# Optimization experiments

Measured on AMD Instinct MI355X. Metric: run time of the kernel, lower is better.

Reference implementation:

```python
import jax, jax.numpy as jnp
import numpy as np

EPS = 1e-5
N = 2097152


def _bn(x, gamma, beta):
    # training-mode BatchNorm1d: biased batch stats over the batch dim
    mean = jnp.mean(x, axis=0)
    var = jnp.var(x, axis=0)
    return (x - mean) * jax.lax.rsqrt(var + EPS) * gamma + beta


def _block(x, W1, g, b, W2, b2):
    # Linear(no bias) -> BN -> ReLU -> Linear(bias)
    h = jax.nn.relu(_bn(x @ W1, g, b))
    return h @ W2 + b2


def setup_inputs() -> dict:
    key = jax.random.key(0)
    ks = jax.random.split(key, 32)
    i = iter(range(32))
    rn = lambda shape, s=0.1: (jax.random.normal(ks[next(i)], shape, dtype=jnp.float32) * s)
    d = {
        "rotation": jax.random.normal(ks[next(i)], (N, 9), dtype=jnp.float32),
        "transition": jax.random.normal(ks[next(i)], (N, 3), dtype=jnp.float32),
        # key net: 3->32 (no bias), BN32, 32->64
        "kW1": rn((3, 32)), "kg": jnp.ones(32), "kb": jnp.zeros(32),
        "kW2": rn((32, 64)), "kb2": rn((64,)),
        # query net: 9->32 (no bias), BN32, 32->64
        "qW1": rn((9, 32)), "qg": jnp.ones(32), "qb": jnp.zeros(32),
        "qW2": rn((32, 64)), "qb2": rn((64,)),
        # value net: 3->32 (no bias), BN32, 32->64
        "vW1": rn((3, 32)), "vg": jnp.ones(32), "vb": jnp.zeros(32),
        "vW2": rn((32, 64)), "vb2": rn((64,)),
        # decoder: 64->32(nb), BN32, ReLU, 32->16(nb), BN16, ReLU, 16->1(b), sigmoid
        "dW1": rn((64, 32)), "dg1": jnp.ones(32), "db1": jnp.zeros(32),
        "dW2": rn((32, 16)), "dg2": jnp.ones(16), "db2": jnp.zeros(16),
        "dW3": rn((16, 1)), "db3": rn((1,)),
    }
    return d


def reference(rotation, transition,
              kW1, kg, kb, kW2, kb2,
              qW1, qg, qb, qW2, qb2,
              vW1, vg, vb, vW2, vb2,
              dW1, dg1, db1, dW2, dg2, db2, dW3, db3):
    k = _block(transition, kW1, kg, kb, kW2, kb2)   # [N, 64]
    q = _block(rotation, qW1, qg, qb, qW2, qb2)     # [N, 64]
    v = _block(transition, vW1, vg, vb, vW2, vb2)   # [N, 64]
    attn = jax.nn.softmax(k * q, axis=-1) * v        # [N, 64]
    h = jax.nn.relu(_bn(attn @ dW1, dg1, db1))       # [N, 32]
    h = jax.nn.relu(_bn(h @ dW2, dg2, db2))          # [N, 16]
    out = jax.nn.sigmoid(h @ dW3 + db3)              # [N, 1]
    return out
```

## Files before the change

kernel.cpp:

```cpp
#include <hip/hip_runtime.h>

#define EPS 1e-5f
#define L2E 1.442695041f

typedef __attribute__((ext_vector_type(8))) short short8;
typedef __attribute__((ext_vector_type(4))) float f32x4;
#define MFMA16(a,b,c) __builtin_amdgcn_mfma_f32_16x16x32_bf16(a,b,c,0,0,0)

typedef float __attribute__((may_alias)) fal;
typedef unsigned short __attribute__((may_alias)) sal;
typedef unsigned int __attribute__((may_alias)) u32al;
typedef uint4 __attribute__((may_alias)) u4al;
typedef f32x4 __attribute__((may_alias)) f4al;

union U8 { short8 s; uint4 u; };

__device__ __forceinline__ float wred(float v){
#pragma unroll
  for(int m=32;m>=1;m>>=1) v += __shfl_xor(v,m,64);
  return v;
}

__device__ __forceinline__ unsigned short f2bf(float f){
  union{unsigned int i; float x;}v; v.x=f;
  unsigned int u=v.i;
  unsigned int r=(u + 0x7fffu + ((u>>16)&1u))>>16;
  return (unsigned short)r;
}
__device__ __forceinline__ unsigned cvtpk(float lo, float hi){
  unsigned r; asm("v_cvt_pk_bf16_f32 %0, %1, %2" : "=v"(r) : "v"(lo), "v"(hi)); return r;
}
__device__ __forceinline__ float bflo(unsigned int u){
  union{unsigned int i; float x;}v; v.i=u<<16; return v.x;
}
__device__ __forceinline__ float bfhi(unsigned int u){
  union{unsigned int i; float x;}v; v.i=u&0xffff0000u; return v.x;
}

__device__ __host__ __forceinline__ int kperm(int k){
  int g=k>>3, e=k&7;
  return (e<4) ? 4*g+e : 16+4*g+(e-4);
}
__device__ __host__ __forceinline__ int kpermD(int kg){
  int kc=kg>>5, kk=kg&31, gm=kk>>3, e=kk&7;
  return 16*(2*kc+(e>>2)) + 4*gm + (e&3);
}

__global__ __launch_bounds__(256) void kT(const float* __restrict__ kW2, const float* __restrict__ qW2,
                                          const float* __restrict__ vW2, const float* __restrict__ dW1,
                                          const float* __restrict__ dW2,
                                          unsigned short* __restrict__ wbf){
  for(int idx=threadIdx.x; idx<2048; idx+=256){
    int k=idx&31, c=idx>>5;
    int f=kperm(k);
    wbf[c*32+k]       = f2bf(kW2[f*64+c]);
    wbf[2048+c*32+k]  = f2bf(qW2[f*64+c]);
    wbf[4096+c*32+k]  = f2bf(vW2[f*64+c]);
  }
  for(int idx=threadIdx.x; idx<2048; idx+=256){
    int f=idx&31, kg=idx>>5;
    wbf[6144 + f*64 + kg] = f2bf(dW1[kpermD(kg)*32 + f]);
  }
  for(int idx=threadIdx.x; idx<512; idx+=256){
    int k=idx>>4, f=idx&15;
    wbf[8192 + f*32 + k] = f2bf(dW2[idx]);
  }
}

__global__ __launch_bounds__(256) void kA(const float* __restrict__ rot, const float* __restrict__ tra,
                                          float* __restrict__ pA, int N){
  float a[63];
#pragma unroll
  for(int i=0;i<63;i++) a[i]=0.f;
  int stride = gridDim.x*blockDim.x;
  for(int row=blockIdx.x*blockDim.x+threadIdx.x; row<N; row+=stride){
    float t[3], r[9];
#pragma unroll
    for(int i=0;i<3;i++) t[i]=tra[row*3+i];
#pragma unroll
    for(int i=0;i<9;i++) r[i]=rot[row*9+i];
#pragma unroll
    for(int i=0;i<3;i++) a[i]+=t[i];
#pragma unroll
    for(int i=0;i<3;i++)
#pragma unroll
      for(int j=i;j<3;j++) a[3 + i*3 - (i*(i-1))/2 + (j-i)] += t[i]*t[j];
#pragma unroll
    for(int i=0;i<9;i++) a[9+i]+=r[i];
#pragma unroll
    for(int i=0;i<9;i++)
#pragma unroll
      for(int j=i;j<9;j++) a[18 + i*9 - (i*(i-1))/2 + (j-i)] += r[i]*r[j];
  }
#pragma unroll
  for(int i=0;i<63;i++) a[i]=wred(a[i]);
  __shared__ __align__(16) float lds[4][63];
  int wave=threadIdx.x>>6, lane=threadIdx.x&63;
  if(lane==0){
#pragma unroll
    for(int i=0;i<63;i++) lds[wave][i]=a[i];
  }
  __syncthreads();
  int t=threadIdx.x;
  if(t<63) pA[t*gridDim.x + blockIdx.x] = lds[0][t]+lds[1][t]+lds[2][t]+lds[3][t];
}

__global__ __launch_bounds__(256) void kA2(const float* __restrict__ pA, int nb,
    const float* __restrict__ kW1, const float* __restrict__ kg, const float* __restrict__ kb,
    const float* __restrict__ qW1, const float* __restrict__ qg, const float* __restrict__ qb,
    const float* __restrict__ vW1, const float* __restrict__ vg, const float* __restrict__ vb,
    float* __restrict__ cst, unsigned short* __restrict__ wA, float invN){
  __shared__ __align__(16) float tmp[63][4];
  __shared__ __align__(16) float mom[63];
  __shared__ __align__(16) float sSc[96];
  __shared__ __align__(16) float sBi[96];
  int t=threadIdx.x;
  if(t<252){
    int f=t>>2, q=t&3;
    int per=nb/4;
    float s=0.f;
    for(int i=0;i<per;i++) s+=pA[f*nb + q*per + i];
    tmp[f][q]=s;
  }
  __syncthreads();
  if(t<63) mom[t]=tmp[t][0]+tmp[t][1]+tmp[t][2]+tmp[t][3];
  __syncthreads();
  if(t<96){
    int net=t>>5, j=t&31;
    const float* W1; const float* g; const float* b; int din, sbase, mbase, obase;
    if(net==0){W1=kW1;g=kg;b=kb;din=3;sbase=0;mbase=3;obase=0;}
    else if(net==1){W1=qW1;g=qg;b=qb;din=9;sbase=9;mbase=18;obase=64;}
    else {W1=vW1;g=vg;b=vb;din=3;sbase=0;mbase=3;obase=128;}
    float mean=0.f, ex2=0.f;
    for(int i=0;i<din;i++){
      float wi=W1[i*32+j];
      mean += mom[sbase+i]*wi;
      int rowb = mbase + i*din - (i*(i-1))/2;
      for(int i2=i;i2<din;i2++){
        float w2=W1[i2*32+j];
        float m=mom[rowb + (i2-i)];
        ex2 += ((i2==i)?1.f:2.f)*wi*w2*m;
      }
    }
    mean*=invN; ex2*=invN;
    float var=ex2-mean*mean;
    float sc=g[j]*rsqrtf(var+EPS);
    float bi=b[j]-mean*sc;
    cst[obase+j]=sc; cst[obase+32+j]=bi;
    sSc[net*32+j]=sc; sBi[net*32+j]=bi;
  }
  __syncthreads();
  for(int i=threadIdx.x; i<3072; i+=256){
    int frag=i>>9, m=(i>>5)&15, k=i&31;
    int net=frag>>1, half=frag&1;
    int f = half*16+m;
    float v=0.f;
    if(net==0){
      if(k<3) v=kW1[k*32+f]*sSc[f];
      else if(k==3) v=sBi[f];
    } else if(net==1){
      if(k>=4 && k<13) v=qW1[(k-4)*32+f]*sSc[32+f];
      else if(k==3) v=sBi[32+f];
    } else {
      if(k<3) v=vW1[k*32+f]*sSc[64+f];
      else if(k==3) v=sBi[64+f];
    }
    wA[i]=f2bf(v);
  }
}

__global__ __launch_bounds__(256) void kRed(const float* __restrict__ part, int nf, int nb,
    const float* __restrict__ g, const float* __restrict__ b, float* __restrict__ cstOut, float invN){
  int f=blockIdx.x;
  float s1=0.f,s2=0.f;
  for(int i=threadIdx.x;i<nb;i+=256){ s1+=part[f*nb+i]; s2+=part[(nf+f)*nb+i]; }
  s1=wred(s1); s2=wred(s2);
  __shared__ __align__(16) float l1[4],l2[4];
  int wave=threadIdx.x>>6;
  if((threadIdx.x&63)==0){l1[wave]=s1;l2[wave]=s2;}
  __syncthreads();
  if(threadIdx.x==0){
    float a=l1[0]+l1[1]+l1[2]+l1[3];
    float c=l2[0]+l2[1]+l2[2]+l2[3];
    float mean=a*invN;
    float var=c*invN-mean*mean;
    float sc=g[f]*rsqrtf(var+EPS);
    float bi=b[f]-mean*sc;
    cstOut[f]=sc; cstOut[nf+f]=bi;
  }
}

__global__ __launch_bounds__(256) void kHeavyM(
    const float* __restrict__ rot, const float* __restrict__ tra,
    const unsigned short* __restrict__ wA, const unsigned short* __restrict__ wbf,
    const float* __restrict__ kb2, const float* __restrict__ qb2, const float* __restrict__ vb2,
    unsigned short* __restrict__ y1o, float* __restrict__ pB, int N, int nb4)
{
  __shared__ __align__(16) unsigned short sbK[2048];
  __shared__ __align__(16) unsigned short sbQ[2048];
  __shared__ __align__(16) unsigned short sbV[2048];
  __shared__ __align__(16) unsigned short sbD[2048];
  __shared__ __align__(16) unsigned short sA[3072];
  __shared__ __align__(16) sal ybuf[4][640];
  for(int i=threadIdx.x;i<2048;i+=256){
    int e=i&7;
    int rK=i>>5, clK=(i>>3)&3;
    int dK = rK*32 + ((clK^(rK&3))<<3) + e;
    sbK[dK]=wbf[i]; sbQ[dK]=wbf[2048+i]; sbV[dK]=wbf[4096+i];
    int rD=i>>6, clD=(i>>3)&7;
    int dD = rD*64 + ((clD^(rD&7))<<3) + e;
    sbD[dD]=wbf[6144+i];
  }
  for(int i=threadIdx.x;i<3072;i+=256){
    int frag=i>>9, m=(i>>5)&15, k=i&31;
    int cl=k>>3, e=k&7;
    sA[frag*512 + m*32 + ((cl^(m&3))<<3) + e] = wA[i];
  }
  int wv=threadIdx.x>>6, lane=threadIdx.x&63;
  int c=lane&15, g=lane>>4;

  f32x4 cK[4],cQ[4],cV[4];
#pragma unroll
  for(int t=0;t<4;t++){
    cK[t]=*(const f4al*)(kb2+16*t+4*g);
    cQ[t]=*(const f4al*)(qb2+16*t+4*g);
    cV[t]=*(const f4al*)(vb2+16*t+4*g);
  }

  float stS0=0.f, stS1=0.f, stQ0=0.f, stQ1=0.f;
  __syncthreads();

  sal* yw = ybuf[wv];
  int wsw = (g^(c&3))<<3;
  f32x4 z4 = {0.f,0.f,0.f,0.f};
  int tileBase = blockIdx.x*1024 + wv*16;

  float pt0,pt1,pt2, pr[9];
  {
    int r0 = tileBase + c;
    int lr = (r0 < N) ? r0 : (N-1);
    pt0=tra[lr*3+0]; pt1=tra[lr*3+1]; pt2=tra[lr*3+2];
#pragma unroll
    for(int i=0;i<9;i++) pr[i]=rot[lr*9+i];
  }

  for(int it=0; it<16; ++it, tileBase += 64){
    if(tileBase >= N) break;
    int row = tileBase + c;
    bool vrow = row < N;

    U8 xB;
    {
      unsigned a0=cvtpk(pt0,pt1), a1=cvtpk(pt2,1.f), a2=cvtpk(pr[0],pr[1]), a3=cvtpk(pr[2],pr[3]);
      unsigned b0=cvtpk(pr[4],pr[5]), b1=cvtpk(pr[6],pr[7]), b2=cvtpk(pr[8],0.f);
      unsigned w0 = (g==0)?a0:((g==1)?b0:0u);
      unsigned w1 = (g==0)?a1:((g==1)?b1:0u);
      unsigned w2 = (g==0)?a2:((g==1)?b2:0u);
      unsigned w3 = (g==0)?a3:0u;
      xB.u = make_uint4(w0,w1,w2,w3);
    }
    {
      int r2 = tileBase + 64 + c;
      int lr2 = (r2 < N) ? r2 : (N-1);
      pt0=tra[lr2*3+0]; pt1=tra[lr2*3+1]; pt2=tra[lr2*3+2];
#pragma unroll
      for(int i=0;i<9;i++) pr[i]=rot[lr2*9+i];
    }

    U8 aK,aQ,aV;
#pragma unroll
    for(int nt=0;nt<3;nt++){
      U8 A1,A2;
      A1.u = *(const u4al*)&sA[(nt*2+0)*512 + c*32 + wsw];
      A2.u = *(const u4al*)&sA[(nt*2+1)*512 + c*32 + wsw];
      f32x4 d1 = MFMA16(A1.s, xB.s, z4);
      f32x4 d2 = MFMA16(A2.s, xB.s, z4);
#pragma unroll
      for(int rg=0;rg<4;rg++){ d1[rg]=fmaxf(d1[rg],0.f); d2[rg]=fmaxf(d2[rg],0.f); }
      uint4 u = make_uint4(cvtpk(d1[0],d1[1]),cvtpk(d1[2],d1[3]),
                           cvtpk(d2[0],d2[1]),cvtpk(d2[2],d2[3]));
      if(nt==0) aK.u=u; else if(nt==1) aQ.u=u; else aV.u=u;
    }

    f32x4 s4[4], av[4];
#pragma unroll
    for(int t=0;t<4;t++){
      U8 bk, bq, bv;
      bk.u = *(const u4al*)&sbK[(t*16+c)*32 + wsw];
      bq.u = *(const u4al*)&sbQ[(t*16+c)*32 + wsw];
      bv.u = *(const u4al*)&sbV[(t*16+c)*32 + wsw];
      f32x4 ak = MFMA16(bk.s, aK.s, cK[t]);
      f32x4 aq = MFMA16(bq.s, aQ.s, cQ[t]);
      av[t]    = MFMA16(bv.s, aV.s, cV[t]);
#pragma unroll
      for(int rg=0;rg<4;rg++) s4[t][rg]=ak[rg]*aq[rg];
    }

    float mx = s4[0][0];
#pragma unroll
    for(int t=0;t<4;t++)
#pragma unroll
      for(int rg=0;rg<4;rg++) mx=fmaxf(mx,s4[t][rg]);
    mx=fmaxf(mx,__shfl_xor(mx,16,64));
    mx=fmaxf(mx,__shfl_xor(mx,32,64));
    float m2 = mx*L2E;
    float zz = 0.f;
#pragma unroll
    for(int t=0;t<4;t++)
#pragma unroll
      for(int rg=0;rg<4;rg++){
        float e = exp2f(fmaf(s4[t][rg], L2E, -m2));
        s4[t][rg]=e; zz+=e;
      }
    zz+=__shfl_xor(zz,16,64);
    zz+=__shfl_xor(zz,32,64);
    float inv = 1.f/zz;

    U8 ap0, ap1;
    {
      float p[4][4];
#pragma unroll
      for(int t=0;t<4;t++)
#pragma unroll
        for(int rg=0;rg<4;rg++) p[t][rg]=s4[t][rg]*inv*av[t][rg];
      ap0.u = make_uint4(cvtpk(p[0][0],p[0][1]),cvtpk(p[0][2],p[0][3]),
                         cvtpk(p[1][0],p[1][1]),cvtpk(p[1][2],p[1][3]));
      ap1.u = make_uint4(cvtpk(p[2][0],p[2][1]),cvtpk(p[2][2],p[2][3]),
                         cvtpk(p[3][0],p[3][1]),cvtpk(p[3][2],p[3][3]));
    }

    f32x4 acy0=z4, acy1=z4;
#pragma unroll
    for(int kc=0;kc<2;kc++){
      int dsw = ((kc*4+g)^(c&7))<<3;
      U8 b0, b1;
      b0.u = *(const u4al*)&sbD[c*64 + dsw];
      b1.u = *(const u4al*)&sbD[(16+c)*64 + dsw];
      acy0 = MFMA16((kc?ap1:ap0).s, b0.s, acy0);
      acy1 = MFMA16((kc?ap1:ap0).s, b1.s, acy1);
    }
#pragma unroll
    for(int rg=0;rg<4;rg++){
      if(tileBase + 4*g + rg >= N){ acy0[rg]=0.f; acy1[rg]=0.f; }
    }
#pragma unroll
    for(int rg=0;rg<4;rg++){
      stS0+=acy0[rg]; stQ0+=acy0[rg]*acy0[rg];
      stS1+=acy1[rg]; stQ1+=acy1[rg]*acy1[rg];
    }
#pragma unroll
    for(int rg=0;rg<4;rg++){
      int m=4*g+rg;
      unsigned pr2 = cvtpk(acy0[rg], acy1[rg]);
      yw[m*40 + c]      = (unsigned short)pr2;
      yw[m*40 + 16 + c] = (unsigned short)(pr2>>16);
    }
    {
      u4al vv = *(const u4al*)&yw[c*40 + 8*g];
      if(vrow) *(uint4*)(y1o + (size_t)row*32 + 8*g) = vv;
    }
  }
  stS0+=__shfl_xor(stS0,16,64); stS0+=__shfl_xor(stS0,32,64);
  stS1+=__shfl_xor(stS1,16,64); stS1+=__shfl_xor(stS1,32,64);
  stQ0+=__shfl_xor(stQ0,16,64); stQ0+=__shfl_xor(stQ0,32,64);
  stQ1+=__shfl_xor(stQ1,16,64); stQ1+=__shfl_xor(stQ1,32,64);
  if(g==0){
    int b4 = blockIdx.x*4 + wv;
    pB[c*nb4 + b4]      = stS0;
    pB[(16+c)*nb4 + b4] = stS1;
    pB[(32+c)*nb4 + b4] = stQ0;
    pB[(48+c)*nb4 + b4] = stQ1;
  }
}

__global__ __launch_bounds__(256) void kCM(const unsigned short* __restrict__ y1,
    const float* __restrict__ cst, const unsigned short* __restrict__ wbf,
    unsigned short* __restrict__ y2o, float* __restrict__ pC, int N, int nb){
  __shared__ __align__(16) unsigned short ybuf[4][256];
  __shared__ __align__(16) float sStat[4][32];
  int wv=threadIdx.x>>6, lane=threadIdx.x&63;
  int c=lane&15, g=lane>>4;
  U8 bD2; bD2.u = *(const uint4*)(wbf + 8192 + c*32 + 8*g);
  float sc[8], bi[8];
#pragma unroll
  for(int i=0;i<8;i++){ sc[i]=cst[192+8*g+i]; bi[i]=cst[224+8*g+i]; }
  float stS=0.f, stQ=0.f;
  unsigned short* yb = ybuf[wv];
  int tileBase = blockIdx.x*1024 + wv*16;
  f32x4 z4 = {0.f,0.f,0.f,0.f};
  uint4 w;
  {
    int r0 = tileBase + c;
    int lr = (r0 < N) ? r0 : (N-1);
    w = *(const uint4*)(y1 + (size_t)lr*32 + 8*g);
  }
  for(int it=0; it<16; ++it, tileBase += 64){
    if(tileBase >= N) break;
    int row = tileBase + c;
    bool vrow = row < N;
    uint4 cur = w;
    {
      int r2 = tileBase + 64 + c;
      int lr2 = (r2 < N) ? r2 : (N-1);
      w = *(const uint4*)(y1 + (size_t)lr2*32 + 8*g);
    }
    unsigned wu[4]={cur.x,cur.y,cur.z,cur.w};
    float h[8];
#pragma unroll
    for(int j=0;j<4;j++){ h[2*j]=bflo(wu[j]); h[2*j+1]=bfhi(wu[j]); }
#pragma unroll
    for(int i=0;i<8;i++){ float x=h[i]*sc[i]+bi[i]; h[i]=fmaxf(x,0.f); }
    U8 a;
    a.u = make_uint4(cvtpk(h[0],h[1]),cvtpk(h[2],h[3]),cvtpk(h[4],h[5]),cvtpk(h[6],h[7]));
    f32x4 acc = MFMA16(a.s, bD2.s, z4);
#pragma unroll
    for(int rg=0;rg<4;rg++){
      if(tileBase + 4*g + rg >= N) acc[rg]=0.f;
      stS+=acc[rg]; stQ+=acc[rg]*acc[rg];
    }
#pragma unroll
    for(int rg=0;rg<4;rg++){
      int m=4*g+rg;
      yb[(m*16 + c) ^ ((m&3)<<2)] = f2bf(acc[rg]);
    }
    {
      int idx = (c*16 + 4*g) ^ ((c&3)<<2);
      uint2 vv = *(uint2*)&yb[idx];
      if(vrow) *(uint2*)(y2o + (size_t)row*16 + 4*g) = vv;
    }
  }
  stS+=__shfl_xor(stS,16,64); stS+=__shfl_xor(stS,32,64);
  stQ+=__shfl_xor(stQ,16,64); stQ+=__shfl_xor(stQ,32,64);
  if(g==0){ sStat[wv][c]=stS; sStat[wv][16+c]=stQ; }
  __syncthreads();
  int t=threadIdx.x;
  if(t<32) pC[t*nb + blockIdx.x] = sStat[0][t]+sStat[1][t]+sStat[2][t]+sStat[3][t];
}

__global__ __launch_bounds__(256) void kD(const unsigned short* __restrict__ y2,
    const float* __restrict__ cst, const float* __restrict__ dW3, const float* __restrict__ db3,
    float* __restrict__ outp, int N){
  int row=blockIdx.x*256+threadIdx.x;
  if(row>=N) return;
  const uint4* src=(const uint4*)(y2+(size_t)row*16);
  uint4 q0=src[0],q1=src[1];
  unsigned int w[8]={q0.x,q0.y,q0.z,q0.w,q1.x,q1.y,q1.z,q1.w};
  float o=db3[0];
#pragma unroll
  for(int kk=0;kk<8;kk++){
    float lo=bflo(w[kk])*cst[256+2*kk]+cst[272+2*kk];
    float hi=bfhi(w[kk])*cst[256+2*kk+1]+cst[272+2*kk+1];
    lo=lo>0.f?lo:0.f; hi=hi>0.f?hi:0.f;
    o+=lo*dW3[2*kk]+hi*dW3[2*kk+1];
  }
  outp[row]=1.f/(1.f+__expf(-o));
}

extern "C" void kernel_launch(void* const* d_in, const int* in_sizes, int n_in,
                              void* d_out, int out_size, void* d_ws, size_t ws_size,
                              hipStream_t stream){
  const float* rot=(const float*)d_in[0];
  const float* tra=(const float*)d_in[1];
  const float* kW1=(const float*)d_in[2];
  const float* kg =(const float*)d_in[3];
  const float* kb =(const float*)d_in[4];
  const float* kW2=(const float*)d_in[5];
  const float* kb2=(const float*)d_in[6];
  const float* qW1=(const float*)d_in[7];
  const float* qg =(const float*)d_in[8];
  const float* qb =(const float*)d_in[9];
  const float* qW2=(const float*)d_in[10];
  const float* qb2=(const float*)d_in[11];
  const float* vW1=(const float*)d_in[12];
  const float* vg =(const float*)d_in[13];
  const float* vb =(const float*)d_in[14];
  const float* vW2=(const float*)d_in[15];
  const float* vb2=(const float*)d_in[16];
  const float* dW1=(const float*)d_in[17];
  const float* dg1=(const float*)d_in[18];
  const float* db1=(const float*)d_in[19];
  const float* dW2=(const float*)d_in[20];
  const float* dg2=(const float*)d_in[21];
  const float* db2=(const float*)d_in[22];
  const float* dW3=(const float*)d_in[23];
  const float* db3=(const float*)d_in[24];

  int N=in_sizes[0]/9;
  int nbH=(N+1023)/1024;
  int nb4=4*nbH;

  float* ws=(float*)d_ws;
  float* cst=ws;
  float* pA =ws+1024;
  float* pB =ws+33280;
  float* pC =pB+(size_t)64*nb4;
  unsigned short* wbf=(unsigned short*)(pC+(size_t)32*nbH);
  unsigned short* wA = wbf+8704;

  size_t y1off=(size_t)8<<20;
  unsigned short* y1=(unsigned short*)((char*)d_ws + y1off);
  unsigned short* y2=(unsigned short*)((char*)d_ws + y1off + (size_t)N*64);
  float invN=1.f/(float)N;
  dim3 B(256);

  kT <<<dim3(1),   B,0,stream>>>(kW2,qW2,vW2,dW1,dW2,wbf);
  kA <<<dim3(512), B,0,stream>>>(rot,tra,pA,N);
  kA2<<<dim3(1),   B,0,stream>>>(pA,512,kW1,kg,kb,qW1,qg,qb,vW1,vg,vb,cst,wA,invN);

  kHeavyM<<<dim3(nbH),B,0,stream>>>(rot,tra,wA,wbf,kb2,qb2,vb2,y1,pB,N,nb4);
  kRed<<<dim3(32),B,0,stream>>>(pB,32,nb4,dg1,db1,cst+192,invN);
  kCM<<<dim3(nbH),B,0,stream>>>(y1,cst,wbf,y2,pC,N,nbH);
  kRed<<<dim3(16),B,0,stream>>>(pC,16,nbH,dg2,db2,cst+256,invN);
  kD <<<dim3((N+255)/256),B,0,stream>>>(y2,cst,dW3,db3,(float*)d_out,N);
}
```

Before: 246.5 us.

## Software-pipeline first-layer MFMAs of next tile and tree-reduce softmax max/sum

Moves the first-layer MFMA computation (input packing plus K/Q/V hidden activations) for the next tile into the current iteration, placed between the second-layer MFMAs and the softmax. The goal is to overlap MFMA latency with the VALU-heavy softmax and cut serial dependency chains. The softmax max and sum reductions become balanced trees instead of linear chains, and the decoder-layer LDS loads are all issued before their MFMAs. The cost is higher register pressure from carrying the next tile's activations across iterations.

```diff
diff --git a/kernel.cpp b/kernel.cpp
--- a/kernel.cpp
+++ b/kernel.cpp
@@ -235,39 +235,21 @@
   f32x4 z4 = {0.f,0.f,0.f,0.f};
   int tileBase = blockIdx.x*1024 + wv*16;
 
-  float pt0,pt1,pt2, pr[9];
+  U8 aK,aQ,aV;
   {
     int r0 = tileBase + c;
     int lr = (r0 < N) ? r0 : (N-1);
-    pt0=tra[lr*3+0]; pt1=tra[lr*3+1]; pt2=tra[lr*3+2];
-#pragma unroll
-    for(int i=0;i<9;i++) pr[i]=rot[lr*9+i];
-  }
-
-  for(int it=0; it<16; ++it, tileBase += 64){
-    if(tileBase >= N) break;
-    int row = tileBase + c;
-    bool vrow = row < N;
-
+    float t0=tra[lr*3+0], t1=tra[lr*3+1], t2=tra[lr*3+2];
+    float r9[9];
+#pragma unroll
+    for(int i=0;i<9;i++) r9[i]=rot[lr*9+i];
     U8 xB;
-    {
-      unsigned a0=cvtpk(pt0,pt1), a1=cvtpk(pt2,1.f), a2=cvtpk(pr[0],pr[1]), a3=cvtpk(pr[2],pr[3]);
-      unsigned b0=cvtpk(pr[4],pr[5]), b1=cvtpk(pr[6],pr[7]), b2=cvtpk(pr[8],0.f);
-      unsigned w0 = (g==0)?a0:((g==1)?b0:0u);
-      unsigned w1 = (g==0)?a1:((g==1)?b1:0u);
-      unsigned w2 = (g==0)?a2:((g==1)?b2:0u);
-      unsigned w3 = (g==0)?a3:0u;
-      xB.u = make_uint4(w0,w1,w2,w3);
-    }
-    {
-      int r2 = tileBase + 64 + c;
-      int lr2 = (r2 < N) ? r2 : (N-1);
-      pt0=tra[lr2*3+0]; pt1=tra[lr2*3+1]; pt2=tra[lr2*3+2];
-#pragma unroll
-      for(int i=0;i<9;i++) pr[i]=rot[lr2*9+i];
-    }
-
-    U8 aK,aQ,aV;
+    unsigned a0=cvtpk(t0,t1), a1=cvtpk(t2,1.f), a2=cvtpk(r9[0],r9[1]), a3=cvtpk(r9[2],r9[3]);
+    unsigned b0=cvtpk(r9[4],r9[5]), b1=cvtpk(r9[6],r9[7]), b2=cvtpk(r9[8],0.f);
+    xB.u = make_uint4((g==0)?a0:((g==1)?b0:0u),
+                      (g==0)?a1:((g==1)?b1:0u),
+                      (g==0)?a2:((g==1)?b2:0u),
+                      (g==0)?a3:0u);
 #pragma unroll
     for(int nt=0;nt<3;nt++){
       U8 A1,A2;
@@ -280,6 +262,21 @@
       uint4 u = make_uint4(cvtpk(d1[0],d1[1]),cvtpk(d1[2],d1[3]),
                            cvtpk(d2[0],d2[1]),cvtpk(d2[2],d2[3]));
       if(nt==0) aK.u=u; else if(nt==1) aQ.u=u; else aV.u=u;
+    }
+  }
+
+  for(int it=0; it<16; ++it, tileBase += 64){
+    if(tileBase >= N) break;
+    int row = tileBase + c;
+    bool vrow = row < N;
+
+    float nt0,nt1,nt2, nr[9];
+    {
+      int r2 = tileBase + 64 + c;
+      int lr2 = (r2 < N) ? r2 : (N-1);
+      nt0=tra[lr2*3+0]; nt1=tra[lr2*3+1]; nt2=tra[lr2*3+2];
+#pragma unroll
+      for(int i=0;i<9;i++) nr[i]=rot[lr2*9+i];
     }
 
     f32x4 s4[4], av[4];
@@ -296,22 +293,54 @@
       for(int rg=0;rg<4;rg++) s4[t][rg]=ak[rg]*aq[rg];
     }
 
-    float mx = s4[0][0];
-#pragma unroll
-    for(int t=0;t<4;t++)
-#pragma unroll
-      for(int rg=0;rg<4;rg++) mx=fmaxf(mx,s4[t][rg]);
+    U8 aKn,aQn,aVn;
+    {
+      U8 xB;
+      unsigned a0=cvtpk(nt0,nt1), a1=cvtpk(nt2,1.f), a2=cvtpk(nr[0],nr[1]), a3=cvtpk(nr[2],nr[3]);
+      unsigned b0=cvtpk(nr[4],nr[5]), b1=cvtpk(nr[6],nr[7]), b2=cvtpk(nr[8],0.f);
+      xB.u = make_uint4((g==0)?a0:((g==1)?b0:0u),
+                        (g==0)?a1:((g==1)?b1:0u),
+                        (g==0)?a2:((g==1)?b2:0u),
+                        (g==0)?a3:0u);
+#pragma unroll
+      for(int nt=0;nt<3;nt++){
+        U8 A1,A2;
+        A1.u = *(const u4al*)&sA[(nt*2+0)*512 + c*32 + wsw];
+        A2.u = *(const u4al*)&sA[(nt*2+1)*512 + c*32 + wsw];
+        f32x4 d1 = MFMA16(A1.s, xB.s, z4);
+        f32x4 d2 = MFMA16(A2.s, xB.s, z4);
+#pragma unroll
+        for(int rg=0;rg<4;rg++){ d1[rg]=fmaxf(d1[rg],0.f); d2[rg]=fmaxf(d2[rg],0.f); }
+        uint4 u = make_uint4(cvtpk(d1[0],d1[1]),cvtpk(d1[2],d1[3]),
+                             cvtpk(d2[0],d2[1]),cvtpk(d2[2],d2[3]));
+        if(nt==0) aKn.u=u; else if(nt==1) aQn.u=u; else aVn.u=u;
+      }
+    }
+
+    float m0,m1,m2_,m3,m4,m5,m6,m7;
+    m0=fmaxf(s4[0][0],s4[0][1]); m1=fmaxf(s4[0][2],s4[0][3]);
+    m2_=fmaxf(s4[1][0],s4[1][1]); m3=fmaxf(s4[1][2],s4[1][3]);
+    m4=fmaxf(s4[2][0],s4[2][1]); m5=fmaxf(s4[2][2],s4[2][3]);
+    m6=fmaxf(s4[3][0],s4[3][1]); m7=fmaxf(s4[3][2],s4[3][3]);
+    m0=fmaxf(m0,m1); m2_=fmaxf(m2_,m3); m4=fmaxf(m4,m5); m6=fmaxf(m6,m7);
+    m0=fmaxf(m0,m2_); m4=fmaxf(m4,m6);
+    float mx=fmaxf(m0,m4);
     mx=fmaxf(mx,__shfl_xor(mx,16,64));
     mx=fmaxf(mx,__shfl_xor(mx,32,64));
     float m2 = mx*L2E;
-    float zz = 0.f;
+    float ee[16];
 #pragma unroll
     for(int t=0;t<4;t++)
 #pragma unroll
       for(int rg=0;rg<4;rg++){
         float e = exp2f(fmaf(s4[t][rg], L2E, -m2));
-        s4[t][rg]=e; zz+=e;
+        s4[t][rg]=e; ee[t*4+rg]=e;
       }
+#pragma unroll
+    for(int i=0;i<8;i++) ee[i]+=ee[i+8];
+#pragma unroll
+    for(int i=0;i<4;i++) ee[i]+=ee[i+4];
+    float zz=(ee[0]+ee[1])+(ee[2]+ee[3]);
     zz+=__shfl_xor(zz,16,64);
     zz+=__shfl_xor(zz,32,64);
     float inv = 1.f/zz;
@@ -330,14 +359,18 @@
     }
 
     f32x4 acy0=z4, acy1=z4;
-#pragma unroll
-    for(int kc=0;kc<2;kc++){
-      int dsw = ((kc*4+g)^(c&7))<<3;
-      U8 b0, b1;
-      b0.u = *(const u4al*)&sbD[c*64 + dsw];
-      b1.u = *(const u4al*)&sbD[(16+c)*64 + dsw];
-      acy0 = MFMA16((kc?ap1:ap0).s, b0.s, acy0);
-      acy1 = MFMA16((kc?ap1:ap0).s, b1.s, acy1);
+    {
+      int dsw0 = ((0*4+g)^(c&7))<<3;
+      int dsw1 = ((1*4+g)^(c&7))<<3;
+      U8 b00,b01,b10,b11;
+      b00.u = *(const u4al*)&sbD[c*64 + dsw0];
+      b01.u = *(const u4al*)&sbD[(16+c)*64 + dsw0];
+      b10.u = *(const u4al*)&sbD[c*64 + dsw1];
+      b11.u = *(const u4al*)&sbD[(16+c)*64 + dsw1];
+      acy0 = MFMA16(ap0.s, b00.s, acy0);
+      acy1 = MFMA16(ap0.s, b01.s, acy1);
+      acy0 = MFMA16(ap1.s, b10.s, acy0);
+      acy1 = MFMA16(ap1.s, b11.s, acy1);
     }
 #pragma unroll
     for(int rg=0;rg<4;rg++){
@@ -359,6 +392,8 @@
       u4al vv = *(const u4al*)&yw[c*40 + 8*g];
       if(vrow) *(uint4*)(y1o + (size_t)row*32 + 8*g) = vv;
     }
+
+    aK=aKn; aQ=aQn; aV=aVn;
   }
   stS0+=__shfl_xor(stS0,16,64); stS0+=__shfl_xor(stS0,32,64);
   stS1+=__shfl_xor(stS1,16,64); stS1+=__shfl_xor(stS1,32,64);
```

New measurement: 267.5 us. 1.09x slower.
